# Kernel tuning notes

Hardware: AMD Instinct MI355X
Metric: run time of the kernel (lower is better)

Reference implementation:

```python
import jax, jax.numpy as jnp
import numpy as np

N_NODES = 100_000
N_EDGES = 1_600_000
HIDDEN = 64
EPS = 1e-5  # eqx.nn.RMSNorm default eps


def setup_inputs() -> dict:
    key = jax.random.key(0)
    k1, k2, k3 = jax.random.split(key, 3)
    x = jax.random.normal(k1, (N_NODES, HIDDEN), dtype=jnp.float32)
    # edges[0] = target node i, edges[1] = source node j  (a[i, j] = 1 => edge j -> i)
    edges = jax.random.randint(k2, (2, N_EDGES), 0, N_NODES, dtype=jnp.int32)
    W = jax.random.normal(k3, (HIDDEN, HIDDEN), dtype=jnp.float32) * (1.0 / np.sqrt(HIDDEN))
    b = jnp.zeros((HIDDEN,), dtype=jnp.float32)
    norm_weight = jnp.ones((HIDDEN,), dtype=jnp.float32)
    norm_bias = jnp.zeros((HIDDEN,), dtype=jnp.float32)
    return {"x": x, "edges": edges, "W": W, "b": b,
            "norm_weight": norm_weight, "norm_bias": norm_bias}


def reference(x, edges, W, b, norm_weight, norm_bias):
    n_nodes = x.shape[0]
    # vmap(Linear) + relu:  m = relu(x @ W.T + b)
    m = jax.nn.relu(jnp.einsum('nd,kd->nk', x, W) + b)
    # a @ m : sum-aggregate messages from source j into target i
    dst, src = edges[0], edges[1]
    agg = jax.ops.segment_sum(m[src], dst, num_segments=n_nodes)
    # residual + RMSNorm (per-node)
    h = x + agg
    inv_rms = jax.lax.rsqrt(jnp.mean(h * h, axis=-1, keepdims=True) + EPS)
    return norm_weight * (h * inv_rms) + norm_bias
```

## Files before the change

kernel.cpp:

```cpp
#include <hip/hip_runtime.h>
#include <hip/hip_bf16.h>

#define N_NODES 100000
#define N_EDGES 1600000
#define HID 64

#define NG 196
#define GROUPS 511
#define GSTRIDE 512
#define NREP 2
#define RCAP 2048
#define EPT 16
#define BIN_BLOCKS 391
#define LIN_BLOCKS 1563
#define LCAP 48

using bf16 = __hip_bfloat16;
typedef __attribute__((ext_vector_type(8))) short short8;
typedef __attribute__((ext_vector_type(4))) float float4v;

__device__ __forceinline__ float bfbits2f(unsigned short u) {
    union { unsigned int i; float f; } v;
    v.i = ((unsigned int)u) << 16;
    return v.f;
}
__device__ __forceinline__ unsigned short f2bfbits(float f) {
    union { float f; unsigned int i; } v;
    v.f = f;
    unsigned int r = v.i + 0x7fffu + ((v.i >> 16) & 1u);
    return (unsigned short)(r >> 16);
}

__global__ __launch_bounds__(256) void k_init(
    const float* __restrict__ W, int* __restrict__ gcur,
    unsigned short* __restrict__ Whi, unsigned short* __restrict__ Wlo)
{
    const int t = blockIdx.x * 256 + threadIdx.x;
    for (int i = t; i < NREP * GSTRIDE; i += 512) gcur[i] = 0;
    for (int i = t; i < HID * HID; i += 512) {
        const float f = W[i];
        const unsigned short h = f2bfbits(f);
        Whi[i] = h;
        Wlo[i] = f2bfbits(f - bfbits2f(h));
    }
}

__global__ __launch_bounds__(256, 4) void k_prep2(
    const float* __restrict__ x, const unsigned short* __restrict__ Whi,
    const unsigned short* __restrict__ Wlo, const float* __restrict__ b,
    bf16* __restrict__ m,
    const int* __restrict__ edges, int* __restrict__ gcur,
    int* __restrict__ binned)
{
    const int t = threadIdx.x;

    if (blockIdx.x < LIN_BLOCKS) {
        const int wv = t >> 6, l = t & 63;
        const int c = l & 15, q = l >> 4;
        const int tile = blockIdx.x * 4 + wv;
        if (tile >= N_NODES / 16) return;
        const int nb = tile * 16;

        const short8* whi8 = reinterpret_cast<const short8*>(Whi);
        const short8* wlo8 = reinterpret_cast<const short8*>(Wlo);
        short8 Bhi[4][2], Blo[4][2];
        #pragma unroll
        for (int nt = 0; nt < 4; ++nt)
            #pragma unroll
            for (int ks = 0; ks < 2; ++ks) {
                const int fi = (nt * 16 + c) * 8 + ks * 4 + q;
                Bhi[nt][ks] = whi8[fi];
                Blo[nt][ks] = wlo8[fi];
            }

        const float* xrow = x + (size_t)(nb + c) * HID;
        short8 Ahi[2];
        #pragma unroll
        for (int ks = 0; ks < 2; ++ks)
            #pragma unroll
            for (int j = 0; j < 8; ++j)
                Ahi[ks][j] = (short)f2bfbits(xrow[ks * 32 + q * 8 + j]);

        float4v acc[4];
        #pragma unroll
        for (int nt = 0; nt < 4; ++nt) {
            const float bias = b[nt * 16 + c];
            acc[nt] = (float4v){bias, bias, bias, bias};
            #pragma unroll
            for (int ks = 0; ks < 2; ++ks) {
                acc[nt] = __builtin_amdgcn_mfma_f32_16x16x32_bf16(Ahi[ks], Bhi[nt][ks], acc[nt], 0, 0, 0);
                acc[nt] = __builtin_amdgcn_mfma_f32_16x16x32_bf16(Ahi[ks], Blo[nt][ks], acc[nt], 0, 0, 0);
            }
        }

        unsigned short* mp = reinterpret_cast<unsigned short*>(m);
        #pragma unroll
        for (int nt = 0; nt < 4; ++nt)
            #pragma unroll
            for (int rg = 0; rg < 4; ++rg) {
                const float v = fmaxf(acc[nt][rg], 0.0f);
                mp[(size_t)(nb + q * 4 + rg) * HID + nt * 16 + c] = f2bfbits(v);
            }
    } else {
        __shared__ int cnt[GSTRIDE];
        __shared__ int base[GSTRIDE];
        const int bb = blockIdx.x - LIN_BLOCKS;
        for (int i = t; i < GSTRIDE; i += 256) cnt[i] = 0;
        __syncthreads();

        const int e0 = bb * (256 * EPT);
        int gk[EPT], pk[EPT], sl[EPT];
        #pragma unroll
        for (int k = 0; k < EPT; ++k) {
            const int e = e0 + k * 256 + t;
            if (e < N_EDGES) {
                const int dst = edges[e];
                const int src = edges[N_EDGES + e];
                const int g = (int)((unsigned)dst / NG);
                gk[k] = g;
                pk[k] = ((dst - g * NG) << 17) | src;
                sl[k] = atomicAdd(&cnt[g], 1);
            } else gk[k] = -1;
        }
        __syncthreads();
        const int r = bb & (NREP - 1);
        for (int i = t; i < GROUPS; i += 256) {
            const int cc = cnt[i];
            base[i] = cc ? atomicAdd(&gcur[r * GSTRIDE + i], cc) : 0;
        }
        __syncthreads();
        #pragma unroll
        for (int k = 0; k < EPT; ++k) {
            if (gk[k] >= 0) {
                const int pos = base[gk[k]] + sl[k];
                if ((unsigned)pos < RCAP)
                    binned[(size_t)(r * GSTRIDE + gk[k]) * RCAP + pos] = pk[k];
            }
        }
    }
}

__global__ __launch_bounds__(1024, 8) void k_gather_norm6(
    const float* __restrict__ x, const bf16* __restrict__ m,
    const int* __restrict__ gcur, const int* __restrict__ binned,
    const float* __restrict__ nw, const float* __restrict__ nb,
    float* __restrict__ out)
{
    __shared__ int lcount[NG];
    __shared__ int lsrc[NG * LCAP];
    const int t = threadIdx.x;
    const int g = blockIdx.x;
    for (int i = t; i < NG; i += 1024) lcount[i] = 0;
    __syncthreads();

    #pragma unroll
    for (int rr = 0; rr < NREP; ++rr) {
        int c = gcur[rr * GSTRIDE + g];
        if (c > RCAP) c = RCAP;
        const int* reg = binned + (size_t)(rr * GSTRIDE + g) * RCAP;
        for (int i = t; i < c; i += 1024) {
            const int pr = reg[i];
            const int dl = pr >> 17;
            const int slot = atomicAdd(&lcount[dl], 1);
            if (slot < LCAP) lsrc[dl * LCAP + slot] = pr & 0x1FFFF;
        }
    }
    __syncthreads();

    const int wv = t >> 6, l = t & 63;
    const int c = l & 15;
    const int r = l >> 4;
    const ushort4* mu4 = reinterpret_cast<const ushort4*>(m);
    const float4 nw4 = reinterpret_cast<const float4*>(nw)[c];
    const float4 nb4 = reinterpret_cast<const float4*>(nb)[c];

    for (int dl = wv; dl < NG; dl += 16) {
        const int n = g * NG + dl;
        if (n >= N_NODES) break;
        int deg = lcount[dl]; if (deg > LCAP) deg = LCAP;
        const int* row = &lsrc[dl * LCAP];

        float4 a = make_float4(0.f, 0.f, 0.f, 0.f);
        for (int i0 = 0; i0 < deg; i0 += 32) {
            ushort4 vb[8];
            #pragma unroll
            for (int j = 0; j < 8; ++j) {
                const int e = i0 + j * 4 + r;
                const int ec = (e < deg) ? e : (deg - 1);
                vb[j] = mu4[(size_t)row[ec] * 16 + c];
            }
            #pragma unroll
            for (int j = 0; j < 8; ++j) {
                const int e = i0 + j * 4 + r;
                if (e < deg) {
                    a.x += bfbits2f(vb[j].x);
                    a.y += bfbits2f(vb[j].y);
                    a.z += bfbits2f(vb[j].z);
                    a.w += bfbits2f(vb[j].w);
                }
            }
        }
        a.x += __shfl_xor(a.x, 16, 64); a.x += __shfl_xor(a.x, 32, 64);
        a.y += __shfl_xor(a.y, 16, 64); a.y += __shfl_xor(a.y, 32, 64);
        a.z += __shfl_xor(a.z, 16, 64); a.z += __shfl_xor(a.z, 32, 64);
        a.w += __shfl_xor(a.w, 16, 64); a.w += __shfl_xor(a.w, 32, 64);

        const float4 x4 = reinterpret_cast<const float4*>(x)[(size_t)n * 16 + c];
        float4 h;
        h.x = x4.x + a.x; h.y = x4.y + a.y; h.z = x4.z + a.z; h.w = x4.w + a.w;
        float ss = h.x * h.x + h.y * h.y + h.z * h.z + h.w * h.w;
        ss += __shfl_xor(ss, 1, 64);
        ss += __shfl_xor(ss, 2, 64);
        ss += __shfl_xor(ss, 4, 64);
        ss += __shfl_xor(ss, 8, 64);
        const float inv = rsqrtf(ss * (1.0f / HID) + 1e-5f);
        if (r == 0) {
            float4 o;
            o.x = nw4.x * h.x * inv + nb4.x;
            o.y = nw4.y * h.y * inv + nb4.y;
            o.z = nw4.z * h.z * inv + nb4.z;
            o.w = nw4.w * h.w * inv + nb4.w;
            reinterpret_cast<float4*>(out)[(size_t)n * 16 + c] = o;
        }
    }
}

extern "C" void kernel_launch(void* const* d_in, const int* in_sizes, int n_in,
                              void* d_out, int out_size, void* d_ws, size_t ws_size,
                              hipStream_t stream) {
    const float* x     = (const float*)d_in[0];
    const int*   edges = (const int*)d_in[1];
    const float* W     = (const float*)d_in[2];
    const float* b     = (const float*)d_in[3];
    const float* nw    = (const float*)d_in[4];
    const float* nb    = (const float*)d_in[5];
    float* out = (float*)d_out;

    int* gcur = (int*)d_ws;
    unsigned short* Whi = (unsigned short*)((char*)d_ws + (1 << 14));
    unsigned short* Wlo = Whi + HID * HID;
    int*  binned = (int*)((char*)d_ws + (1 << 16));
    bf16* m      = (bf16*)((char*)d_ws + (1 << 16) +
                           (size_t)NREP * GSTRIDE * RCAP * sizeof(int));

    k_init<<<2, 256, 0, stream>>>(W, gcur, Whi, Wlo);
    k_prep2<<<LIN_BLOCKS + BIN_BLOCKS, 256, 0, stream>>>(x, Whi, Wlo, b, m, edges, gcur, binned);
    k_gather_norm6<<<GROUPS, 1024, 0, stream>>>(x, m, gcur, binned, nw, nb, out);
}
```

Before: 156.0 us.

## Halve node groups per block and widen gather loads to 16-byte rows

Doubles the number of destination groups (98 nodes each, 512-thread blocks) so more, smaller blocks run the gather. Each lane now loads a uint4 of 8 bf16 values per edge instead of 4, with 8 lanes covering a row. The aim is better load balance across CUs and fewer, wider gather transactions. The per-group capacity drops to 1024, which raises overflow risk if a group's edge count exceeds it. The unseen binning kernel must also derive the group index from NG for results to stay correct.

Result: slower. 160.5 us (+2.9%).

```diff
diff --git a/kernel.cpp b/kernel.cpp
--- a/kernel.cpp
+++ b/kernel.cpp
@@ -5,11 +5,11 @@
 #define N_EDGES 1600000
 #define HID 64
 
-#define NG 196
-#define GROUPS 511
-#define GSTRIDE 512
+#define NG 98
+#define GROUPS 1021
+#define GSTRIDE 1024
 #define NREP 2
-#define RCAP 2048
+#define RCAP 1024
 #define EPT 16
 #define BIN_BLOCKS 391
 #define LIN_BLOCKS 1563
@@ -29,6 +29,12 @@
     v.f = f;
     unsigned int r = v.i + 0x7fffu + ((v.i >> 16) & 1u);
     return (unsigned short)(r >> 16);
+}
+__device__ __forceinline__ void unpack_bf2(unsigned int u, float& lo, float& hi) {
+    union { unsigned int i; float f; } a, b;
+    a.i = u << 16;
+    b.i = u & 0xffff0000u;
+    lo = a.f; hi = b.f;
 }
 
 __global__ __launch_bounds__(256) void k_init(
@@ -140,7 +146,7 @@
     }
 }
 
-__global__ __launch_bounds__(1024, 8) void k_gather_norm6(
+__global__ __launch_bounds__(512, 8) void k_gather_norm7(
     const float* __restrict__ x, const bf16* __restrict__ m,
     const int* __restrict__ gcur, const int* __restrict__ binned,
     const float* __restrict__ nw, const float* __restrict__ nb,
@@ -150,15 +156,15 @@
     __shared__ int lsrc[NG * LCAP];
     const int t = threadIdx.x;
     const int g = blockIdx.x;
-    for (int i = t; i < NG; i += 1024) lcount[i] = 0;
+    for (int i = t; i < NG; i += 512) lcount[i] = 0;
     __syncthreads();
 
     #pragma unroll
     for (int rr = 0; rr < NREP; ++rr) {
-        int c = gcur[rr * GSTRIDE + g];
-        if (c > RCAP) c = RCAP;
+        int cc = gcur[rr * GSTRIDE + g];
+        if (cc > RCAP) cc = RCAP;
         const int* reg = binned + (size_t)(rr * GSTRIDE + g) * RCAP;
-        for (int i = t; i < c; i += 1024) {
+        for (int i = t; i < cc; i += 512) {
             const int pr = reg[i];
             const int dl = pr >> 17;
             const int slot = atomicAdd(&lcount[dl], 1);
@@ -168,59 +174,72 @@
     __syncthreads();
 
     const int wv = t >> 6, l = t & 63;
-    const int c = l & 15;
-    const int r = l >> 4;
-    const ushort4* mu4 = reinterpret_cast<const ushort4*>(m);
-    const float4 nw4 = reinterpret_cast<const float4*>(nw)[c];
-    const float4 nb4 = reinterpret_cast<const float4*>(nb)[c];
-
-    for (int dl = wv; dl < NG; dl += 16) {
+    const int c = l & 7;
+    const int r = l >> 3;
+    const uint4* mu4 = reinterpret_cast<const uint4*>(m);
+
+    for (int dl = wv; dl < NG; dl += 8) {
         const int n = g * NG + dl;
         if (n >= N_NODES) break;
         int deg = lcount[dl]; if (deg > LCAP) deg = LCAP;
         const int* row = &lsrc[dl * LCAP];
 
-        float4 a = make_float4(0.f, 0.f, 0.f, 0.f);
+        float a[8] = {0.f, 0.f, 0.f, 0.f, 0.f, 0.f, 0.f, 0.f};
         for (int i0 = 0; i0 < deg; i0 += 32) {
-            ushort4 vb[8];
-            #pragma unroll
-            for (int j = 0; j < 8; ++j) {
-                const int e = i0 + j * 4 + r;
+            uint4 vb[4];
+            #pragma unroll
+            for (int j = 0; j < 4; ++j) {
+                const int e = i0 + j * 8 + r;
                 const int ec = (e < deg) ? e : (deg - 1);
-                vb[j] = mu4[(size_t)row[ec] * 16 + c];
-            }
-            #pragma unroll
-            for (int j = 0; j < 8; ++j) {
-                const int e = i0 + j * 4 + r;
+                vb[j] = mu4[(size_t)row[ec] * 8 + c];
+            }
+            #pragma unroll
+            for (int j = 0; j < 4; ++j) {
+                const int e = i0 + j * 8 + r;
                 if (e < deg) {
-                    a.x += bfbits2f(vb[j].x);
-                    a.y += bfbits2f(vb[j].y);
-                    a.z += bfbits2f(vb[j].z);
-                    a.w += bfbits2f(vb[j].w);
+                    float lo, hi;
+                    unpack_bf2(vb[j].x, lo, hi); a[0] += lo; a[1] += hi;
+                    unpack_bf2(vb[j].y, lo, hi); a[2] += lo; a[3] += hi;
+                    unpack_bf2(vb[j].z, lo, hi); a[4] += lo; a[5] += hi;
+                    unpack_bf2(vb[j].w, lo, hi); a[6] += lo; a[7] += hi;
                 }
             }
         }
-        a.x += __shfl_xor(a.x, 16, 64); a.x += __shfl_xor(a.x, 32, 64);
-        a.y += __shfl_xor(a.y, 16, 64); a.y += __shfl_xor(a.y, 32, 64);
-        a.z += __shfl_xor(a.z, 16, 64); a.z += __shfl_xor(a.z, 32, 64);
-        a.w += __shfl_xor(a.w, 16, 64); a.w += __shfl_xor(a.w, 32, 64);
-
-        const float4 x4 = reinterpret_cast<const float4*>(x)[(size_t)n * 16 + c];
-        float4 h;
-        h.x = x4.x + a.x; h.y = x4.y + a.y; h.z = x4.z + a.z; h.w = x4.w + a.w;
-        float ss = h.x * h.x + h.y * h.y + h.z * h.z + h.w * h.w;
+        #pragma unroll
+        for (int f = 0; f < 8; ++f) {
+            a[f] += __shfl_xor(a[f], 8, 64);
+            a[f] += __shfl_xor(a[f], 16, 64);
+            a[f] += __shfl_xor(a[f], 32, 64);
+        }
+
+        const float4 xa = reinterpret_cast<const float4*>(x)[(size_t)n * 16 + c * 2];
+        const float4 xb = reinterpret_cast<const float4*>(x)[(size_t)n * 16 + c * 2 + 1];
+        float h[8];
+        h[0] = xa.x + a[0]; h[1] = xa.y + a[1]; h[2] = xa.z + a[2]; h[3] = xa.w + a[3];
+        h[4] = xb.x + a[4]; h[5] = xb.y + a[5]; h[6] = xb.z + a[6]; h[7] = xb.w + a[7];
+        float ss = 0.f;
+        #pragma unroll
+        for (int f = 0; f < 8; ++f) ss += h[f] * h[f];
         ss += __shfl_xor(ss, 1, 64);
         ss += __shfl_xor(ss, 2, 64);
         ss += __shfl_xor(ss, 4, 64);
-        ss += __shfl_xor(ss, 8, 64);
         const float inv = rsqrtf(ss * (1.0f / HID) + 1e-5f);
         if (r == 0) {
-            float4 o;
-            o.x = nw4.x * h.x * inv + nb4.x;
-            o.y = nw4.y * h.y * inv + nb4.y;
-            o.z = nw4.z * h.z * inv + nb4.z;
-            o.w = nw4.w * h.w * inv + nb4.w;
-            reinterpret_cast<float4*>(out)[(size_t)n * 16 + c] = o;
+            const float4 nwa = reinterpret_cast<const float4*>(nw)[c * 2];
+            const float4 nwb = reinterpret_cast<const float4*>(nw)[c * 2 + 1];
+            const float4 nba = reinterpret_cast<const float4*>(nb)[c * 2];
+            const float4 nbb = reinterpret_cast<const float4*>(nb)[c * 2 + 1];
+            float4 oa, ob;
+            oa.x = nwa.x * h[0] * inv + nba.x;
+            oa.y = nwa.y * h[1] * inv + nba.y;
+            oa.z = nwa.z * h[2] * inv + nba.z;
+            oa.w = nwa.w * h[3] * inv + nba.w;
+            ob.x = nwb.x * h[4] * inv + nbb.x;
+            ob.y = nwb.y * h[5] * inv + nbb.y;
+            ob.z = nwb.z * h[6] * inv + nbb.z;
+            ob.w = nwb.w * h[7] * inv + nbb.w;
+            reinterpret_cast<float4*>(out)[(size_t)n * 16 + c * 2] = oa;
+            reinterpret_cast<float4*>(out)[(size_t)n * 16 + c * 2 + 1] = ob;
         }
     }
 }
@@ -245,5 +264,5 @@
 
     k_init<<<2, 256, 0, stream>>>(W, gcur, Whi, Wlo);
     k_prep2<<<LIN_BLOCKS + BIN_BLOCKS, 256, 0, stream>>>(x, Whi, Wlo, b, m, edges, gcur, binned);
-    k_gather_norm6<<<GROUPS, 1024, 0, stream>>>(x, m, gcur, binned, nw, nb, out);
-}
+    k_gather_norm7<<<GROUPS, 512, 0, stream>>>(x, m, gcur, binned, nw, nb, out);
+}
```
